# Kernel tuning notes

Measured on AMD Instinct MI355X. Metric: run time of the kernel, lower is better.

Reference implementation:

```python
import jax, jax.numpy as jnp
import numpy as np

D = 16      # stroke_embedding_dim
H = 2       # num_heads
DH = D // H # head dim = 8
HID = 32    # hidden_dim
OUT = 32    # output_dim
N = 250000  # num edge nodes
F = 500000  # num faces
E = 4       # edges per face


def setup_inputs() -> dict:
    key = jax.random.key(0)
    ks = jax.random.split(key, 10)
    s = 1.0 / np.sqrt(D)
    return {
        "node_embed": jax.random.normal(ks[0], (1, N, D), dtype=jnp.float32),
        "face_edge_ids": jax.random.randint(ks[1], (F, E), 0, N),
        # nn.MultiheadAttention in_proj (packed q,k,v) and out_proj, stored [in, out]
        "w_in": jax.random.uniform(ks[2], (D, 3 * D), jnp.float32, -s, s),
        "b_in": jnp.zeros((3 * D,), jnp.float32),
        "w_out": jax.random.uniform(ks[3], (D, D), jnp.float32, -s, s),
        "b_out": jnp.zeros((D,), jnp.float32),
        # fc: Linear(16 -> 32), fc_output: Linear(32 -> 32)
        "fc_w": jax.random.uniform(ks[4], (D, HID), jnp.float32, -s, s),
        "fc_b": jax.random.uniform(ks[5], (HID,), jnp.float32, -s, s),
        "fco_w": jax.random.uniform(ks[6], (HID, OUT), jnp.float32, -1 / np.sqrt(HID), 1 / np.sqrt(HID)),
        "fco_b": jax.random.uniform(ks[7], (OUT,), jnp.float32, -1 / np.sqrt(HID), 1 / np.sqrt(HID)),
    }


def reference(node_embed, face_edge_ids, w_in, b_in, w_out, b_out, fc_w, fc_b, fco_w, fco_b):
    # Gather per-face edge embeddings: [F, E, D]
    x = node_embed[0][face_edge_ids]
    # Packed qkv projection
    qkv = x @ w_in + b_in                                  # [F, E, 3D]
    q, k, v = jnp.split(qkv, 3, axis=-1)
    def heads(t):
        return t.reshape(F, E, H, DH).transpose(0, 2, 1, 3)  # [F, H, E, DH]
    q, k, v = heads(q), heads(k), heads(v)
    scores = jnp.einsum("fhqd,fhkd->fhqk", q, k) / np.sqrt(DH)
    attn = jax.nn.softmax(scores, axis=-1)
    o = jnp.einsum("fhqk,fhkd->fhqd", attn, v)             # [F, H, E, DH]
    o = o.transpose(0, 2, 1, 3).reshape(F, E, D)
    attn_out = o @ w_out + b_out                           # [F, E, D]
    h = jax.nn.relu(attn_out @ fc_w + fc_b)                # [F, E, HID]
    pooled = h.mean(axis=1)                                # [F, HID]
    out = pooled @ fco_w + fco_b                           # [F, OUT]
    return out[None]                                       # [1, F, OUT]
```

## Files before the change

kernel.cpp:

```cpp
#include <hip/hip_runtime.h>
#include <stdint.h>


typedef float v2f __attribute__((ext_vector_type(2)));
typedef _Float16 v2h __attribute__((ext_vector_type(2)));

#define DPP_ROT1 0x39
#define DPP_ROT2 0x4E
#define DPP_ROT3 0x93
#define DPP_XOR1 0xB1

template<int CTRL>
static __device__ __forceinline__ float dppf(float x) {
    return __builtin_bit_cast(float,
        __builtin_amdgcn_mov_dpp(__builtin_bit_cast(int, x), CTRL, 0xF, 0xF, true));
}
template<int CTRL>
static __device__ __forceinline__ v2h dpph(v2h x) {
    return __builtin_bit_cast(v2h,
        __builtin_amdgcn_mov_dpp(__builtin_bit_cast(int, x), CTRL, 0xF, 0xF, true));
}

static __device__ __forceinline__ v2h pkh(float a, float b) {
    v2h r; r.x = (_Float16)a; r.y = (_Float16)b; return r;
}
static __device__ __forceinline__ v2h pkrtz(float a, float b) {
#if __has_builtin(__builtin_amdgcn_cvt_pkrtz)
    return __builtin_bit_cast(v2h, __builtin_amdgcn_cvt_pkrtz(a, b));
#else
    return pkh(a, b);
#endif
}
static __device__ __forceinline__ float fdot2(v2h a, v2h b, float c) {
#if __has_builtin(__builtin_amdgcn_fdot2)
    return __builtin_amdgcn_fdot2(a, b, c, false);
#else
    return fmaf((float)a.x, (float)b.x, fmaf((float)a.y, (float)b.y, c));
#endif
}
static __device__ __forceinline__ v2h fmah(v2h a, v2h b, v2h c) {
    return __builtin_elementwise_fma(a, b, c);
}
static __device__ __forceinline__ v2h ldh2(const uint32_t* p) {
    return __builtin_bit_cast(v2h, *p);
}
static __device__ __forceinline__ v2h ash(uint32_t u) {
    return __builtin_bit_cast(v2h, u);
}

template<int CTRL>
static __device__ __forceinline__ void score_rot(const v2h* qh, const v2h* kh,
                                                 float& r0, float& r1) {
    float a0 = 0.f, a1 = 0.f;
#pragma unroll
    for (int d = 0; d < 4; ++d) {
        a0 = fdot2(qh[d],     dpph<CTRL>(kh[d]),     a0);
        a1 = fdot2(qh[4 + d], dpph<CTRL>(kh[4 + d]), a1);
    }
    r0 = a0; r1 = a1;
}

template<int CTRL>
static __device__ __forceinline__ void pv_rot(const v2h* vh, v2h ps0, v2h ps1,
                                              v2h* o) {
#pragma unroll
    for (int d = 0; d < 8; ++d) {
        const v2h vr = dpph<CTRL>(vh[d]);
        o[d] = fmah(d < 4 ? ps0 : ps1, vr, o[d]);
    }
}

__global__ void fold_w(const float* __restrict__ w_in,
                       const float* __restrict__ w_out,
                       const float* __restrict__ b_out,
                       const float* __restrict__ fc_w,
                       const float* __restrict__ fc_b,
                       const float* __restrict__ fco_w,
                       uint32_t* __restrict__ wsu) {
    const int tid = threadIdx.x;
    if (blockIdx.x == 1) {
        if (tid < 512) {
            const int j = tid >> 5, col = tid & 31;
            wsu[672 + tid] = __builtin_bit_cast(uint32_t,
                pkh(fco_w[(2 * j) * 32 + col] * 0.25f,
                    fco_w[(2 * j + 1) * 32 + col] * 0.25f));
        }
        return;
    }
    if (tid < 384) {
        const int o = tid >> 3, p = tid & 7;
        const v2h h = pkh(w_in[(2 * p) * 48 + o], w_in[(2 * p + 1) * 48 + o]);
        wsu[tid] = __builtin_bit_cast(uint32_t, h);
    } else if (tid < 640) {
        const int i = tid - 384, c = i >> 3, p = i & 7;
        float a0 = 0.f, a1 = 0.f;
#pragma unroll
        for (int e = 0; e < 16; ++e) {
            a0 = fmaf(w_out[(2 * p) * 16 + e],     fc_w[e * 32 + c], a0);
            a1 = fmaf(w_out[(2 * p + 1) * 16 + e], fc_w[e * 32 + c], a1);
        }
        wsu[tid] = __builtin_bit_cast(uint32_t, pkh(a0, a1));
    } else if (tid < 672) {
        const int c = tid - 640;
        float acc = fc_b[c];
#pragma unroll
        for (int e = 0; e < 16; ++e)
            acc = fmaf(b_out[e], fc_w[e * 32 + c], acc);
        reinterpret_cast<float*>(wsu)[640 + c] = acc;
    }
}

__launch_bounds__(256, 3)
__global__ void face_net(const float* __restrict__ node,
                         const int*   __restrict__ fids,
                         const float* __restrict__ b_in,
                         const uint32_t* __restrict__ wsu,
                         const float* __restrict__ fco_b,
                         float* __restrict__ out, int F) {
    const int g = blockIdx.x * 256 + threadIdx.x;
    const int f = g >> 2;
    if (f >= F) return;
    const int t = g & 3;
    const int t8 = t * 8;

    const int nid = fids[g];
    const float* xp = node + (size_t)nid * 16;
    const float4 xv0 = *reinterpret_cast<const float4*>(xp);
    const float4 xv1 = *reinterpret_cast<const float4*>(xp + 4);
    const float4 xv2 = *reinterpret_cast<const float4*>(xp + 8);
    const float4 xv3 = *reinterpret_cast<const float4*>(xp + 12);
    v2h xh[8];
    xh[0] = pkrtz(xv0.x, xv0.y); xh[1] = pkrtz(xv0.z, xv0.w);
    xh[2] = pkrtz(xv1.x, xv1.y); xh[3] = pkrtz(xv1.z, xv1.w);
    xh[4] = pkrtz(xv2.x, xv2.y); xh[5] = pkrtz(xv2.z, xv2.w);
    xh[6] = pkrtz(xv3.x, xv3.y); xh[7] = pkrtz(xv3.z, xv3.w);

    float qa[16], ka[16], va[16];
#pragma unroll
    for (int o = 0; o < 16; ++o) {
        float aq = b_in[o], ak = 0.f, av = b_in[32 + o];
        const uint32_t* wq = wsu + o * 8;
        const uint32_t* wk = wsu + (16 + o) * 8;
        const uint32_t* wv = wsu + (32 + o) * 8;
#pragma unroll
        for (int p = 0; p < 8; ++p) {
            aq = fdot2(xh[p], ldh2(wq + p), aq);
            ak = fdot2(xh[p], ldh2(wk + p), ak);
            av = fdot2(xh[p], ldh2(wv + p), av);
        }
        qa[o] = aq; ka[o] = ak; va[o] = av;
    }

    v2h qh[8], kh[8], vh[8];
#pragma unroll
    for (int i = 0; i < 8; ++i) {
        qh[i] = pkrtz(qa[2 * i], qa[2 * i + 1]);
        kh[i] = pkrtz(ka[2 * i], ka[2 * i + 1]);
        vh[i] = pkrtz(va[2 * i], va[2 * i + 1]);
    }

    float p0[4], p1[4];
    {
        float a0 = 0.f, a1 = 0.f;
#pragma unroll
        for (int d = 0; d < 4; ++d) {
            a0 = fdot2(qh[d], kh[d], a0);
            a1 = fdot2(qh[4 + d], kh[4 + d], a1);
        }
        p0[0] = a0; p1[0] = a1;
    }
    score_rot<DPP_ROT1>(qh, kh, p0[1], p1[1]);
    score_rot<DPP_ROT2>(qh, kh, p0[2], p1[2]);
    score_rot<DPP_ROT3>(qh, kh, p0[3], p1[3]);

    {
        const float C = 0.51006974841f;
        float s0 = 0.f, s1 = 0.f;
#pragma unroll
        for (int j = 0; j < 4; ++j) {
            p0[j] = __builtin_amdgcn_exp2f(p0[j] * C); s0 += p0[j];
            p1[j] = __builtin_amdgcn_exp2f(p1[j] * C); s1 += p1[j];
        }
        const float r0 = __builtin_amdgcn_rcpf(s0);
        const float r1 = __builtin_amdgcn_rcpf(s1);
#pragma unroll
        for (int j = 0; j < 4; ++j) { p0[j] *= r0; p1[j] *= r1; }
    }

    v2h ps0[4], ps1[4];
#pragma unroll
    for (int r = 0; r < 4; ++r) {
        ps0[r] = pkrtz(p0[r], p0[r]);
        ps1[r] = pkrtz(p1[r], p1[r]);
    }

    v2h o[8];
#pragma unroll
    for (int d = 0; d < 4; ++d) {
        o[d]     = ps0[0] * vh[d];
        o[4 + d] = ps1[0] * vh[4 + d];
    }
    pv_rot<DPP_ROT1>(vh, ps0[1], ps1[1], o);
    pv_rot<DPP_ROT2>(vh, ps0[2], ps1[2], o);
    pv_rot<DPP_ROT3>(vh, ps0[3], ps1[3], o);

    const uint32_t* w1t = wsu + 384;
    const float* b1 = reinterpret_cast<const float*>(wsu) + 640;
    const uint32_t* wd = wsu + 672 + t8;
    float acc[8];
    {
        const float4 ob0 = *reinterpret_cast<const float4*>(fco_b + t8);
        const float4 ob1 = *reinterpret_cast<const float4*>(fco_b + t8 + 4);
        acc[0] = ob0.x; acc[1] = ob0.y; acc[2] = ob0.z; acc[3] = ob0.w;
        acc[4] = ob1.x; acc[5] = ob1.y; acc[6] = ob1.z; acc[7] = ob1.w;
    }
#pragma unroll 4
    for (int j = 0; j < 16; ++j) {
        const uint32_t* wr0 = w1t + (2 * j) * 8;
        const uint32_t* wr1 = w1t + (2 * j + 1) * 8;
        float a0 = b1[2 * j], a1 = b1[2 * j + 1];
#pragma unroll
        for (int p = 0; p < 8; ++p) {
            a0 = fdot2(o[p], ldh2(wr0 + p), a0);
            a1 = fdot2(o[p], ldh2(wr1 + p), a1);
        }
        float h0 = fmaxf(a0, 0.f), h1 = fmaxf(a1, 0.f);
        float s0 = h0 + dppf<DPP_XOR1>(h0); s0 = s0 + dppf<DPP_ROT2>(s0);
        float s1 = h1 + dppf<DPP_XOR1>(h1); s1 = s1 + dppf<DPP_ROT2>(s1);
        const v2h ph = pkrtz(s0, s1);
        const uint4 wa = *reinterpret_cast<const uint4*>(wd + j * 32);
        const uint4 wb = *reinterpret_cast<const uint4*>(wd + j * 32 + 4);
        acc[0] = fdot2(ph, ash(wa.x), acc[0]);
        acc[1] = fdot2(ph, ash(wa.y), acc[1]);
        acc[2] = fdot2(ph, ash(wa.z), acc[2]);
        acc[3] = fdot2(ph, ash(wa.w), acc[3]);
        acc[4] = fdot2(ph, ash(wb.x), acc[4]);
        acc[5] = fdot2(ph, ash(wb.y), acc[5]);
        acc[6] = fdot2(ph, ash(wb.z), acc[6]);
        acc[7] = fdot2(ph, ash(wb.w), acc[7]);
    }

    float* op = out + (size_t)f * 32 + t8;
    *reinterpret_cast<float4*>(op)     = make_float4(acc[0], acc[1], acc[2], acc[3]);
    *reinterpret_cast<float4*>(op + 4) = make_float4(acc[4], acc[5], acc[6], acc[7]);
}

extern "C" void kernel_launch(void* const* d_in, const int* in_sizes, int n_in,
                              void* d_out, int out_size, void* d_ws, size_t ws_size,
                              hipStream_t stream) {
    const float* node  = (const float*)d_in[0];
    const int*   fids  = (const int*)  d_in[1];
    const float* w_in  = (const float*)d_in[2];
    const float* b_in  = (const float*)d_in[3];
    const float* w_out = (const float*)d_in[4];
    const float* b_out = (const float*)d_in[5];
    const float* fc_w  = (const float*)d_in[6];
    const float* fc_b  = (const float*)d_in[7];
    const float* fco_w = (const float*)d_in[8];
    const float* fco_b = (const float*)d_in[9];
    float* out = (float*)d_out;
    uint32_t* wsu = (uint32_t*)d_ws;
    const int F = in_sizes[1] / 4;

    hipLaunchKernelGGL(fold_w, dim3(2), dim3(672), 0, stream,
                       w_in, w_out, b_out, fc_w, fc_b, fco_w, wsu);
    const int threads = F * 4;
    const int blocks = (threads + 255) / 256;
    hipLaunchKernelGGL(face_net, dim3(blocks), dim3(256), 0, stream,
                       node, fids, b_in, wsu, fco_b, out, F);
}
```

Before: 162.2 us.

## Move QKV, hidden and output projections onto 16x16x16 f16 MFMA with LDS transposes

Replaces the per-thread fdot2 projections (QKV, folded out_proj+fc, and fc_output) with 16x16x16 f16 MFMA instructions per wavefront. Weights are pre-packed in the fold kernel into the MFMA B-operand layout, and results are exchanged through per-wave LDS scratch to get back to the per-token layout that the DPP attention code expects. Mean pooling is done inside the MFMA output fragment before the final projection. Occupancy hint rises to 4 blocks. This adds LDS traffic and shuffles, plus relies on wavefront-local data without barriers. The aim is to cut VALU instruction count.

```diff
diff --git a/kernel.cpp b/kernel.cpp
--- a/kernel.cpp
+++ b/kernel.cpp
@@ -4,6 +4,10 @@
 
 typedef float v2f __attribute__((ext_vector_type(2)));
 typedef _Float16 v2h __attribute__((ext_vector_type(2)));
+typedef __fp16 h4 __attribute__((ext_vector_type(4)));
+typedef float f32x4 __attribute__((ext_vector_type(4)));
+typedef uint32_t u32x2 __attribute__((ext_vector_type(2)));
+typedef uint32_t u32x4 __attribute__((ext_vector_type(4)));
 
 #define DPP_ROT1 0x39
 #define DPP_ROT2 0x4E
@@ -41,11 +45,20 @@
 static __device__ __forceinline__ v2h fmah(v2h a, v2h b, v2h c) {
     return __builtin_elementwise_fma(a, b, c);
 }
-static __device__ __forceinline__ v2h ldh2(const uint32_t* p) {
-    return __builtin_bit_cast(v2h, *p);
-}
 static __device__ __forceinline__ v2h ash(uint32_t u) {
     return __builtin_bit_cast(v2h, u);
+}
+static __device__ __forceinline__ uint32_t bcu(v2h h) {
+    return __builtin_bit_cast(uint32_t, h);
+}
+static __device__ __forceinline__ h4 mkh4(uint32_t lo, uint32_t hi) {
+    u32x2 t; t.x = lo; t.y = hi; return __builtin_bit_cast(h4, t);
+}
+static __device__ __forceinline__ h4 ld2h(const uint32_t* p) {
+    u32x2 t; t.x = p[0]; t.y = p[1]; return __builtin_bit_cast(h4, t);
+}
+static __device__ __forceinline__ f32x4 mfma16(h4 a, h4 b, f32x4 c) {
+    return __builtin_amdgcn_mfma_f32_16x16x16f16(a, b, c, 0, 0, 0);
 }
 
 template<int CTRL>
@@ -59,7 +72,6 @@
     }
     r0 = a0; r1 = a1;
 }
-
 template<int CTRL>
 static __device__ __forceinline__ void pv_rot(const v2h* vh, v2h ps0, v2h ps1,
                                               v2h* o) {
@@ -67,6 +79,22 @@
     for (int d = 0; d < 8; ++d) {
         const v2h vr = dpph<CTRL>(vh[d]);
         o[d] = fmah(d < 4 ? ps0 : ps1, vr, o[d]);
+    }
+}
+
+static __device__ __forceinline__ void xchg_store(uint32_t* S, int a, int c0,
+                                                  int g2, f32x4 c) {
+    const float p0 = dppf<DPP_XOR1>(c[0]);
+    const float p1 = dppf<DPP_XOR1>(c[1]);
+    const float p2 = dppf<DPP_XOR1>(c[2]);
+    const float p3 = dppf<DPP_XOR1>(c[3]);
+    if ((c0 & 1) == 0) {
+        u32x4 w;
+        w.x = bcu(pkrtz(c[0], p0));
+        w.y = bcu(pkrtz(c[1], p1));
+        w.z = bcu(pkrtz(c[2], p2));
+        w.w = bcu(pkrtz(c[3], p3));
+        *reinterpret_cast<u32x4*>(S + ((c0 >> 1) * 68 + 16 * a + 4 * g2)) = w;
     }
 }
 
@@ -78,85 +106,86 @@
                        const float* __restrict__ fco_w,
                        uint32_t* __restrict__ wsu) {
     const int tid = threadIdx.x;
-    if (blockIdx.x == 1) {
-        if (tid < 512) {
-            const int j = tid >> 5, col = tid & 31;
-            wsu[672 + tid] = __builtin_bit_cast(uint32_t,
-                pkh(fco_w[(2 * j) * 32 + col] * 0.25f,
-                    fco_w[(2 * j + 1) * 32 + col] * 0.25f));
-        }
-        return;
-    }
-    if (tid < 384) {
-        const int o = tid >> 3, p = tid & 7;
-        const v2h h = pkh(w_in[(2 * p) * 48 + o], w_in[(2 * p + 1) * 48 + o]);
-        wsu[tid] = __builtin_bit_cast(uint32_t, h);
-    } else if (tid < 640) {
-        const int i = tid - 384, c = i >> 3, p = i & 7;
-        float a0 = 0.f, a1 = 0.f;
-#pragma unroll
-        for (int e = 0; e < 16; ++e) {
-            a0 = fmaf(w_out[(2 * p) * 16 + e],     fc_w[e * 32 + c], a0);
-            a1 = fmaf(w_out[(2 * p + 1) * 16 + e], fc_w[e * 32 + c], a1);
-        }
-        wsu[tid] = __builtin_bit_cast(uint32_t, pkh(a0, a1));
-    } else if (tid < 672) {
-        const int c = tid - 640;
-        float acc = fc_b[c];
-#pragma unroll
-        for (int e = 0; e < 16; ++e)
-            acc = fmaf(b_out[e], fc_w[e * 32 + c], acc);
-        reinterpret_cast<float*>(wsu)[640 + c] = acc;
-    }
-}
-
-__launch_bounds__(256, 3)
+    if (blockIdx.x == 0) {
+        if (tid < 384) {
+            const int T = tid >> 7, r = tid & 127, l = r >> 1, d = r & 1;
+            const int o = 16 * T + (l & 15), k0 = 4 * (l >> 4) + 2 * d;
+            wsu[tid] = bcu(pkh(w_in[k0 * 48 + o], w_in[(k0 + 1) * 48 + o]));
+        } else if (tid < 640) {
+            const int i = tid - 384, b = i >> 7, r = i & 127, l = r >> 1, d = r & 1;
+            const int c = 16 * b + (l & 15), k0 = 4 * (l >> 4) + 2 * d;
+            float a0 = 0.f, a1 = 0.f;
+#pragma unroll
+            for (int e = 0; e < 16; ++e) {
+                a0 = fmaf(w_out[k0 * 16 + e],       fc_w[e * 32 + c], a0);
+                a1 = fmaf(w_out[(k0 + 1) * 16 + e], fc_w[e * 32 + c], a1);
+            }
+            wsu[tid] = bcu(pkh(a0, a1));
+        }
+    } else {
+        if (tid < 32) {
+            float acc = fc_b[tid];
+#pragma unroll
+            for (int e = 0; e < 16; ++e)
+                acc = fmaf(b_out[e], fc_w[e * 32 + tid], acc);
+            reinterpret_cast<float*>(wsu)[640 + tid] = acc;
+        } else if (tid < 544) {
+            const int i = tid - 32;
+            const int kt = i >> 8, n = (i >> 7) & 1, r = i & 127, l = r >> 1, d = r & 1;
+            const int col = 16 * n + (l & 15), k0 = 16 * kt + 4 * (l >> 4) + 2 * d;
+            wsu[672 + i] = bcu(pkh(fco_w[k0 * 32 + col] * 0.25f,
+                                   fco_w[(k0 + 1) * 32 + col] * 0.25f));
+        }
+    }
+}
+
+__launch_bounds__(256, 4)
 __global__ void face_net(const float* __restrict__ node,
                          const int*   __restrict__ fids,
                          const float* __restrict__ b_in,
                          const uint32_t* __restrict__ wsu,
                          const float* __restrict__ fco_b,
                          float* __restrict__ out, int F) {
-    const int g = blockIdx.x * 256 + threadIdx.x;
-    const int f = g >> 2;
-    if (f >= F) return;
-    const int t = g & 3;
-    const int t8 = t * 8;
-
-    const int nid = fids[g];
-    const float* xp = node + (size_t)nid * 16;
-    const float4 xv0 = *reinterpret_cast<const float4*>(xp);
-    const float4 xv1 = *reinterpret_cast<const float4*>(xp + 4);
-    const float4 xv2 = *reinterpret_cast<const float4*>(xp + 8);
-    const float4 xv3 = *reinterpret_cast<const float4*>(xp + 12);
-    v2h xh[8];
-    xh[0] = pkrtz(xv0.x, xv0.y); xh[1] = pkrtz(xv0.z, xv0.w);
-    xh[2] = pkrtz(xv1.x, xv1.y); xh[3] = pkrtz(xv1.z, xv1.w);
-    xh[4] = pkrtz(xv2.x, xv2.y); xh[5] = pkrtz(xv2.z, xv2.w);
-    xh[6] = pkrtz(xv3.x, xv3.y); xh[7] = pkrtz(xv3.z, xv3.w);
-
-    float qa[16], ka[16], va[16];
-#pragma unroll
-    for (int o = 0; o < 16; ++o) {
-        float aq = b_in[o], ak = 0.f, av = b_in[32 + o];
-        const uint32_t* wq = wsu + o * 8;
-        const uint32_t* wk = wsu + (16 + o) * 8;
-        const uint32_t* wv = wsu + (32 + o) * 8;
-#pragma unroll
-        for (int p = 0; p < 8; ++p) {
-            aq = fdot2(xh[p], ldh2(wq + p), aq);
-            ak = fdot2(xh[p], ldh2(wk + p), ak);
-            av = fdot2(xh[p], ldh2(wv + p), av);
-        }
-        qa[o] = aq; ka[o] = ak; va[o] = av;
-    }
-
-    v2h qh[8], kh[8], vh[8];
-#pragma unroll
-    for (int i = 0; i < 8; ++i) {
-        qh[i] = pkrtz(qa[2 * i], qa[2 * i + 1]);
-        kh[i] = pkrtz(ka[2 * i], ka[2 * i + 1]);
-        vh[i] = pkrtz(va[2 * i], va[2 * i + 1]);
+    const int l   = threadIdx.x & 63;
+    const int wid = threadIdx.x >> 6;
+    const int token_base = blockIdx.x * 256 + wid * 64;
+    if (token_base >= 4 * F) return;
+    const int c0 = l & 15, g2 = l >> 4;
+
+    __shared__ __align__(16) uint8_t lds[4 * 4736];
+    uint8_t* wl = lds + wid * 4736;
+    uint32_t* S0 = reinterpret_cast<uint32_t*>(wl);
+    uint32_t* S1 = reinterpret_cast<uint32_t*>(wl + 2176);
+
+    h4 A[4];
+#pragma unroll
+    for (int a = 0; a < 4; ++a) {
+        const int tok = token_base + 16 * a + c0;
+        const int nid = fids[tok];
+        const float4 xv = *reinterpret_cast<const float4*>(
+            node + (size_t)nid * 16 + g2 * 4);
+        A[a] = mkh4(bcu(pkrtz(xv.x, xv.y)), bcu(pkrtz(xv.z, xv.w)));
+    }
+
+    const h4 Bq = ld2h(wsu + 0   + l * 2);
+    const h4 Bk = ld2h(wsu + 128 + l * 2);
+    const float bq = b_in[c0];
+    {
+        const f32x4 cq0 = {bq, bq, bq, bq};
+        const f32x4 ck0 = {0.f, 0.f, 0.f, 0.f};
+#pragma unroll
+        for (int a = 0; a < 4; ++a) xchg_store(S0, a, c0, g2, mfma16(A[a], Bq, cq0));
+#pragma unroll
+        for (int a = 0; a < 4; ++a) xchg_store(S1, a, c0, g2, mfma16(A[a], Bk, ck0));
+    }
+
+    v2h qh[8], kh[8];
+#pragma unroll
+    for (int u = 0; u < 4; ++u) {
+        qh[2 * u]     = ash(S0[(2 * u) * 68 + l]);
+        qh[2 * u + 1] = ash(S0[(2 * u + 1) * 68 + l]);
+        kh[2 * u]     = ash(S1[(2 * u) * 68 + l]);
+        kh[2 * u + 1] = ash(S1[(2 * u + 1) * 68 + l]);
     }
 
     float p0[4], p1[4];
@@ -187,13 +216,26 @@
         for (int j = 0; j < 4; ++j) { p0[j] *= r0; p1[j] *= r1; }
     }
 
+    const h4 Bv = ld2h(wsu + 256 + l * 2);
+    const float bv = b_in[32 + c0];
+    {
+        const f32x4 cv0 = {bv, bv, bv, bv};
+#pragma unroll
+        for (int a = 0; a < 4; ++a) xchg_store(S0, a, c0, g2, mfma16(A[a], Bv, cv0));
+    }
+    v2h vh[8];
+#pragma unroll
+    for (int u = 0; u < 4; ++u) {
+        vh[2 * u]     = ash(S0[(2 * u) * 68 + l]);
+        vh[2 * u + 1] = ash(S0[(2 * u + 1) * 68 + l]);
+    }
+
     v2h ps0[4], ps1[4];
 #pragma unroll
     for (int r = 0; r < 4; ++r) {
         ps0[r] = pkrtz(p0[r], p0[r]);
         ps1[r] = pkrtz(p1[r], p1[r]);
     }
-
     v2h o[8];
 #pragma unroll
     for (int d = 0; d < 4; ++d) {
@@ -204,45 +246,70 @@
     pv_rot<DPP_ROT2>(vh, ps0[2], ps1[2], o);
     pv_rot<DPP_ROT3>(vh, ps0[3], ps1[3], o);
 
-    const uint32_t* w1t = wsu + 384;
-    const float* b1 = reinterpret_cast<const float*>(wsu) + 640;
-    const uint32_t* wd = wsu + 672 + t8;
-    float acc[8];
-    {
-        const float4 ob0 = *reinterpret_cast<const float4*>(fco_b + t8);
-        const float4 ob1 = *reinterpret_cast<const float4*>(fco_b + t8 + 4);
-        acc[0] = ob0.x; acc[1] = ob0.y; acc[2] = ob0.z; acc[3] = ob0.w;
-        acc[4] = ob1.x; acc[5] = ob1.y; acc[6] = ob1.z; acc[7] = ob1.w;
-    }
-#pragma unroll 4
-    for (int j = 0; j < 16; ++j) {
-        const uint32_t* wr0 = w1t + (2 * j) * 8;
-        const uint32_t* wr1 = w1t + (2 * j + 1) * 8;
-        float a0 = b1[2 * j], a1 = b1[2 * j + 1];
-#pragma unroll
-        for (int p = 0; p < 8; ++p) {
-            a0 = fdot2(o[p], ldh2(wr0 + p), a0);
-            a1 = fdot2(o[p], ldh2(wr1 + p), a1);
-        }
-        float h0 = fmaxf(a0, 0.f), h1 = fmaxf(a1, 0.f);
-        float s0 = h0 + dppf<DPP_XOR1>(h0); s0 = s0 + dppf<DPP_ROT2>(s0);
-        float s1 = h1 + dppf<DPP_XOR1>(h1); s1 = s1 + dppf<DPP_ROT2>(s1);
-        const v2h ph = pkrtz(s0, s1);
-        const uint4 wa = *reinterpret_cast<const uint4*>(wd + j * 32);
-        const uint4 wb = *reinterpret_cast<const uint4*>(wd + j * 32 + 4);
-        acc[0] = fdot2(ph, ash(wa.x), acc[0]);
-        acc[1] = fdot2(ph, ash(wa.y), acc[1]);
-        acc[2] = fdot2(ph, ash(wa.z), acc[2]);
-        acc[3] = fdot2(ph, ash(wa.w), acc[3]);
-        acc[4] = fdot2(ph, ash(wb.x), acc[4]);
-        acc[5] = fdot2(ph, ash(wb.y), acc[5]);
-        acc[6] = fdot2(ph, ash(wb.z), acc[6]);
-        acc[7] = fdot2(ph, ash(wb.w), acc[7]);
-    }
-
-    float* op = out + (size_t)f * 32 + t8;
-    *reinterpret_cast<float4*>(op)     = make_float4(acc[0], acc[1], acc[2], acc[3]);
-    *reinterpret_cast<float4*>(op + 4) = make_float4(acc[4], acc[5], acc[6], acc[7]);
+#pragma unroll
+    for (int j = 0; j < 4; ++j) {
+        u32x2 w; w.x = bcu(o[2 * j]); w.y = bcu(o[2 * j + 1]);
+        *reinterpret_cast<u32x2*>(S1 + l * 10 + 2 * j) = w;
+    }
+    h4 Ao[4];
+#pragma unroll
+    for (int a = 0; a < 4; ++a) {
+        const u32x2 t = *reinterpret_cast<const u32x2*>(
+            S1 + (16 * a + c0) * 10 + 2 * g2);
+        Ao[a] = __builtin_bit_cast(h4, t);
+    }
+
+    const h4 Bh0 = ld2h(wsu + 384 + l * 2);
+    const h4 Bh1 = ld2h(wsu + 384 + 128 + l * 2);
+    const float* b1f = reinterpret_cast<const float*>(wsu) + 640;
+    const float b10 = b1f[c0], b11 = b1f[16 + c0];
+    float* Pf = reinterpret_cast<float*>(S0);
+    {
+        const f32x4 ch0 = {b10, b10, b10, b10};
+        const f32x4 ch1 = {b11, b11, b11, b11};
+#pragma unroll
+        for (int a = 0; a < 4; ++a) {
+            const f32x4 h0 = mfma16(Ao[a], Bh0, ch0);
+            const f32x4 h1 = mfma16(Ao[a], Bh1, ch1);
+            const float s0 = fmaxf(h0[0], 0.f) + fmaxf(h0[1], 0.f)
+                           + fmaxf(h0[2], 0.f) + fmaxf(h0[3], 0.f);
+            const float s1 = fmaxf(h1[0], 0.f) + fmaxf(h1[1], 0.f)
+                           + fmaxf(h1[2], 0.f) + fmaxf(h1[3], 0.f);
+            Pf[(4 * a + g2) * 34 + c0]      = s0;
+            Pf[(4 * a + g2) * 34 + 16 + c0] = s1;
+        }
+    }
+
+    h4 Af[2];
+#pragma unroll
+    for (int kt = 0; kt < 2; ++kt) {
+        const u32x2 pa = *reinterpret_cast<const u32x2*>(
+            S0 + c0 * 34 + 16 * kt + 4 * g2);
+        const u32x2 pb = *reinterpret_cast<const u32x2*>(
+            S0 + c0 * 34 + 16 * kt + 4 * g2 + 2);
+        const v2f fa = __builtin_bit_cast(v2f, pa);
+        const v2f fb = __builtin_bit_cast(v2f, pb);
+        Af[kt] = mkh4(bcu(pkrtz(fa.x, fa.y)), bcu(pkrtz(fb.x, fb.y)));
+    }
+    const h4 Bf00 = ld2h(wsu + 672 + 0 * 128 + l * 2);
+    const h4 Bf01 = ld2h(wsu + 672 + 1 * 128 + l * 2);
+    const h4 Bf10 = ld2h(wsu + 672 + 2 * 128 + l * 2);
+    const h4 Bf11 = ld2h(wsu + 672 + 3 * 128 + l * 2);
+    const float fb0 = fco_b[c0], fb1 = fco_b[16 + c0];
+    f32x4 cf0 = {fb0, fb0, fb0, fb0};
+    f32x4 cf1 = {fb1, fb1, fb1, fb1};
+    cf0 = mfma16(Af[0], Bf00, cf0);
+    cf0 = mfma16(Af[1], Bf10, cf0);
+    cf1 = mfma16(Af[0], Bf01, cf1);
+    cf1 = mfma16(Af[1], Bf11, cf1);
+
+    const int fbase = token_base >> 2;
+    float* ob = out + (size_t)(fbase + 4 * g2) * 32 + c0;
+#pragma unroll
+    for (int r = 0; r < 4; ++r) {
+        ob[r * 32]      = cf0[r];
+        ob[r * 32 + 16] = cf1[r];
+    }
 }
 
 extern "C" void kernel_launch(void* const* d_in, const int* in_sizes, int n_in,
@@ -262,7 +329,7 @@
     uint32_t* wsu = (uint32_t*)d_ws;
     const int F = in_sizes[1] / 4;
 
-    hipLaunchKernelGGL(fold_w, dim3(2), dim3(672), 0, stream,
+    hipLaunchKernelGGL(fold_w, dim3(2), dim3(640), 0, stream,
                        w_in, w_out, b_out, fc_w, fc_b, fco_w, wsu);
     const int threads = F * 4;
     const int blocks = (threads + 255) / 256;
```

Measured after the change: 134.9 us. 1.2x faster.
